# Kernel optimization log

Measured on AMD Instinct MI355X. Metric: run time of the kernel, lower is better.

The kernel has to match this reference:

```python
import jax, jax.numpy as jnp
import numpy as np

B, N_AGENTS, EMBED, HID, N_ACT, S_DIM, O_DIM = 16384, 32, 32, 64, 5, 512, 256


def setup_inputs() -> dict:
    key = jax.random.key(0)
    ks = jax.random.split(key, 12)
    w = lambda k, s: jax.random.normal(k, s, jnp.float32) * 0.05
    return dict(
        states=jax.random.normal(ks[0], (B, S_DIM), jnp.float32),
        agents_obs=jax.random.normal(ks[1], (B, N_AGENTS, O_DIM), jnp.float32),
        fc1_w=w(ks[2], (O_DIM, HID)), fc1_b=jnp.zeros((HID,), jnp.float32),
        fc2_w=w(ks[3], (HID, N_ACT)), fc2_b=jnp.zeros((N_ACT,), jnp.float32),
        hw1_w=w(ks[4], (S_DIM, EMBED * N_AGENTS)), hw1_b=jnp.zeros((EMBED * N_AGENTS,), jnp.float32),
        hb1_w=w(ks[5], (S_DIM, EMBED)), hb1_b=jnp.zeros((EMBED,), jnp.float32),
        hwf_w=w(ks[6], (S_DIM, EMBED)), hwf_b=jnp.zeros((EMBED,), jnp.float32),
        v1_w=w(ks[7], (S_DIM, EMBED)), v1_b=jnp.zeros((EMBED,), jnp.float32),
        v2_w=w(ks[8], (EMBED, 1)), v2_b=jnp.zeros((1,), jnp.float32),
    )


def reference(states, agents_obs, fc1_w, fc1_b, fc2_w, fc2_b,
              hw1_w, hw1_b, hb1_w, hb1_b, hwf_w, hwf_b,
              v1_w, v1_b, v2_w, v2_b):
    # agent network: per-agent Q values [B, N, A]
    x = jax.nn.relu(agents_obs @ fc1_w + fc1_b)
    agents_qs = jax.nn.softmax(x @ fc2_w + fc2_b, axis=-1)

    Bn = states.shape[0]
    # hypernetwork: per-sample mixing weights (non-negative via abs)
    w1 = jnp.abs(states @ hw1_w + hw1_b).reshape(Bn, N_AGENTS, EMBED)  # [B,N,E]
    b1 = states @ hb1_w + hb1_b                                        # [B,E]
    wf = jnp.abs(states @ hwf_w + hwf_b)                               # [B,E]
    v = jax.nn.relu(states @ v1_w + v1_b) @ v2_w + v2_b                # [B,1]

    # chosen (greedy) per-agent Q values
    best_qs = jnp.max(agents_qs, axis=-1)                              # [B,N]

    # batched mixing (replaces the original per-sample python loop)
    y = jax.nn.relu(jnp.einsum('bn,bne->be', best_qs, w1) + b1)        # [B,E]
    q_tot = jnp.einsum('be,be->b', y, wf) + v[:, 0]                    # [B]
    return agents_qs, q_tot
```

## Files before the change

### kernel.cpp

```cpp
#include <hip/hip_runtime.h>
#include <stdint.h>

#define BTOT   16384
#define ROWS_A 524288
#define WT_COLS 1120

#define WT_OFF    0
#define FC1T_OFF  1146880
#define BQ_OFF    1179648

typedef __attribute__((ext_vector_type(8))) short bf8_t;
typedef __attribute__((ext_vector_type(4))) float f4_t;

__device__ __forceinline__ f4_t mfma16(bf8_t a, bf8_t b, f4_t c) {
    return __builtin_amdgcn_mfma_f32_16x16x32_bf16(a, b, c, 0, 0, 0);
}
__device__ __forceinline__ unsigned short f2bf(float f) {
    union { float f; uint32_t u; } x; x.f = f;
    uint32_t r = x.u + 0x7FFFu + ((x.u >> 16) & 1u);
    return (unsigned short)(r >> 16);
}
__device__ __forceinline__ float bf2f(unsigned short h) {
    union { uint32_t u; float f; } x; x.u = ((uint32_t)h) << 16;
    return x.f;
}

__global__ void prep_kernel(const float* __restrict__ fc1_w,
                            const float* __restrict__ hw1_w,
                            const float* __restrict__ hb1_w,
                            const float* __restrict__ hwf_w,
                            const float* __restrict__ v1_w,
                            unsigned short* __restrict__ Wt,
                            unsigned short* __restrict__ fc1t)
{
    int tid = blockIdx.x * 256 + threadIdx.x;
    if (tid < 71680) {
        int e = tid * 8;
        int c = e >> 9, k0 = e & 511;
        const float* src; int N, sc;
        if (c < 1024)      { src = hw1_w; N = 1024; sc = c; }
        else if (c < 1056) { src = hb1_w; N = 32;   sc = c - 1024; }
        else if (c < 1088) { src = hwf_w; N = 32;   sc = c - 1056; }
        else               { src = v1_w;  N = 32;   sc = c - 1088; }
        union { unsigned short s[8]; uint4 v; } pk;
        #pragma unroll
        for (int j = 0; j < 8; ++j) pk.s[j] = f2bf(src[(size_t)(k0 + j) * N + sc]);
        *(uint4*)(Wt + (size_t)c * 512 + k0) = pk.v;
    } else if (tid < 73728) {
        int e = (tid - 71680) * 8;
        int n = e >> 8, k0 = e & 255;
        union { unsigned short s[8]; uint4 v; } pk;
        #pragma unroll
        for (int j = 0; j < 8; ++j) pk.s[j] = f2bf(fc1_w[(size_t)(k0 + j) * 64 + n]);
        *(uint4*)(fc1t + n * 256 + k0) = pk.v;
    }
}

#define A_SB 264
#define A_SA 72
__global__ __launch_bounds__(256, 3)
void agent_kernel(const float* __restrict__ obs,
                  const unsigned short* __restrict__ fc1t,
                  const float* __restrict__ fc1_b,
                  const float* __restrict__ fc2_w,
                  const float* __restrict__ fc2_b,
                  float* __restrict__ out_q,
                  float* __restrict__ bq)
{
    __shared__ unsigned short sB[64 * A_SB];
    __shared__ unsigned short sA[128 * A_SA];
    const int t = threadIdx.x;
    const int R0 = blockIdx.x * 128;
    const int w = t >> 6, lane = t & 63;
    const int c0 = lane & 15, quad = lane >> 4;

    {
        const uint4* src = (const uint4*)fc1t;
        #pragma unroll
        for (int i = 0; i < 8; ++i) {
            int id = t + i * 256;
            int n = id >> 5, off = (id & 31) * 8;
            *(uint4*)(sB + n * A_SB + off) = src[id];
        }
    }

    f4_t acc[2][4];
    #pragma unroll
    for (int mt = 0; mt < 2; ++mt)
        #pragma unroll
        for (int nt = 0; nt < 4; ++nt) acc[mt][nt] = (f4_t){0.f, 0.f, 0.f, 0.f};

    for (int kc = 0; kc < 4; ++kc) {
        __syncthreads();
        #pragma unroll
        for (int i = 0; i < 8; ++i) {
            int id = t + i * 256;
            int row = id >> 4, off = (id & 15) * 4;
            float4 v = *(const float4*)(obs + (size_t)(R0 + row) * 256 + kc * 64 + off);
            ushort4 o; o.x = f2bf(v.x); o.y = f2bf(v.y); o.z = f2bf(v.z); o.w = f2bf(v.w);
            *(ushort4*)(sA + row * A_SA + off) = o;
        }
        __syncthreads();
        #pragma unroll
        for (int ks = 0; ks < 2; ++ks) {
            int kk = ks * 32 + quad * 8;
            bf8_t af[2], bfr[4];
            af[0] = *(const bf8_t*)(sA + (w * 32 + c0) * A_SA + kk);
            af[1] = *(const bf8_t*)(sA + (w * 32 + 16 + c0) * A_SA + kk);
            #pragma unroll
            for (int nt = 0; nt < 4; ++nt)
                bfr[nt] = *(const bf8_t*)(sB + (nt * 16 + c0) * A_SB + kc * 64 + kk);
            #pragma unroll
            for (int mt = 0; mt < 2; ++mt)
                #pragma unroll
                for (int nt = 0; nt < 4; ++nt)
                    acc[mt][nt] = mfma16(af[mt], bfr[nt], acc[mt][nt]);
        }
    }
    __syncthreads();
    unsigned short* xs = sA;
    #pragma unroll
    for (int nt = 0; nt < 4; ++nt) {
        int col = nt * 16 + c0;
        float bias = fc1_b[col];
        #pragma unroll
        for (int mt = 0; mt < 2; ++mt)
            #pragma unroll
            for (int r = 0; r < 4; ++r) {
                int row = w * 32 + mt * 16 + quad * 4 + r;
                float v = acc[mt][nt][r] + bias;
                xs[row * 66 + col] = f2bf(fmaxf(v, 0.f));
            }
    }
    __syncthreads();
    {
        int row = t >> 1, half = t & 1;
        float q[5] = {0.f, 0.f, 0.f, 0.f, 0.f};
        #pragma unroll
        for (int i = 0; i < 32; ++i) {
            int h = half * 32 + i;
            float xv = bf2f(xs[row * 66 + h]);
            #pragma unroll
            for (int j = 0; j < 5; ++j) q[j] += xv * fc2_w[h * 5 + j];
        }
        #pragma unroll
        for (int j = 0; j < 5; ++j) q[j] = q[j] + __shfl_xor(q[j], 1) + fc2_b[j];
        float m = q[0];
        #pragma unroll
        for (int j = 1; j < 5; ++j) m = fmaxf(m, q[j]);
        float e[5], s = 0.f;
        #pragma unroll
        for (int j = 0; j < 5; ++j) { e[j] = __expf(q[j] - m); s += e[j]; }
        float inv = 1.f / s;
        if (half == 0) {
            size_t G = (size_t)R0 + row;
            #pragma unroll
            for (int j = 0; j < 5; ++j) out_q[G * 5 + j] = e[j] * inv;
            bq[G] = inv;
        }
    }
}

#define B_ST 520
__global__ __launch_bounds__(256, 1)
void mixer_kernel(const float* __restrict__ states,
                  const unsigned short* __restrict__ Wt,
                  const float* __restrict__ hw1_b,
                  const float* __restrict__ hb1_b,
                  const float* __restrict__ hwf_b,
                  const float* __restrict__ v1_b,
                  const float* __restrict__ v2_w,
                  const float* __restrict__ v2_b,
                  const float* __restrict__ bq,
                  float* __restrict__ qtot)
{
    extern __shared__ char smem[];
    unsigned short* sA = (unsigned short*)smem;
    unsigned short* sB = (unsigned short*)(smem + 66560);
    float* bqs = (float*)(smem + 133120);
    const int t = threadIdx.x;
    const int B0 = blockIdx.x * 64;
    const int w = t >> 6, lane = t & 63;
    const int c0 = lane & 15, quad = lane >> 4;

    #pragma unroll
    for (int i = 0; i < 32; ++i) {
        int id = t + i * 256;
        int row = id >> 7, off = (id & 127) * 4;
        float4 v = *(const float4*)(states + (size_t)(B0 + row) * 512 + off);
        ushort4 o; o.x = f2bf(v.x); o.y = f2bf(v.y); o.z = f2bf(v.z); o.w = f2bf(v.w);
        *(ushort4*)(sA + row * B_ST + off) = o;
    }
    #pragma unroll
    for (int i = 0; i < 2; ++i) {
        int id = t + i * 256;
        int row = id >> 3, off = (id & 7) * 4;
        float4 v = *(const float4*)(bq + (size_t)(B0 + row) * 32 + off);
        *(float4*)(bqs + row * 36 + off) = v;
    }

    float y_acc[4][2] = {{0.f,0.f},{0.f,0.f},{0.f,0.f},{0.f,0.f}};
    float b1v[4][2], wfv[4][2], vhv[4][2];

    for (int g = 0; g < 18; ++g) {
        __syncthreads();
        int nrows = (g == 17) ? 32 : 64;
        int n0 = g * 64;
        int nv4 = nrows * 64;
        for (int id = t; id < nv4; id += 256) {
            int n = id >> 6, off = (id & 63) * 8;
            *(uint4*)(sB + n * B_ST + off) = *(const uint4*)(Wt + (size_t)(n0 + n) * 512 + off);
        }
        __syncthreads();
        int NT = (g == 17) ? 2 : 4;
        f4_t acc[4];
        #pragma unroll
        for (int nt = 0; nt < 4; ++nt) acc[nt] = (f4_t){0.f, 0.f, 0.f, 0.f};
        for (int ks = 0; ks < 16; ++ks) {
            int kk = ks * 32 + quad * 8;
            bf8_t af = *(const bf8_t*)(sA + (w * 16 + c0) * B_ST + kk);
            for (int nt = 0; nt < NT; ++nt) {
                bf8_t bfr = *(const bf8_t*)(sB + (nt * 16 + c0) * B_ST + kk);
                acc[nt] = mfma16(af, bfr, acc[nt]);
            }
        }
        if (g < 16) {
            #pragma unroll
            for (int nt = 0; nt < 4; ++nt) {
                int colg = n0 + nt * 16 + c0;
                int agent = colg >> 5;
                int eh = nt & 1;
                float bias = hw1_b[colg];
                #pragma unroll
                for (int r = 0; r < 4; ++r) {
                    int rowl = w * 16 + quad * 4 + r;
                    float w1v = fabsf(acc[nt][r] + bias);
                    y_acc[r][eh] += bqs[rowl * 36 + agent] * w1v;
                }
            }
        } else if (g == 16) {
            #pragma unroll
            for (int nt = 0; nt < 2; ++nt) {
                float bias = hb1_b[nt * 16 + c0];
                #pragma unroll
                for (int r = 0; r < 4; ++r) b1v[r][nt] = acc[nt][r] + bias;
            }
            #pragma unroll
            for (int nt = 2; nt < 4; ++nt) {
                float bias = hwf_b[(nt - 2) * 16 + c0];
                #pragma unroll
                for (int r = 0; r < 4; ++r) wfv[r][nt - 2] = fabsf(acc[nt][r] + bias);
            }
        } else {
            #pragma unroll
            for (int nt = 0; nt < 2; ++nt) {
                float bias = v1_b[nt * 16 + c0];
                #pragma unroll
                for (int r = 0; r < 4; ++r) vhv[r][nt] = fmaxf(acc[nt][r] + bias, 0.f);
            }
        }
    }
    float v2w0 = v2_w[c0], v2w1 = v2_w[16 + c0], v2b = v2_b[0];
    float p[4];
    #pragma unroll
    for (int r = 0; r < 4; ++r) {
        float y0 = fmaxf(y_acc[r][0] + b1v[r][0], 0.f);
        float y1 = fmaxf(y_acc[r][1] + b1v[r][1], 0.f);
        p[r] = y0 * wfv[r][0] + y1 * wfv[r][1] + vhv[r][0] * v2w0 + vhv[r][1] * v2w1;
    }
    #pragma unroll
    for (int off = 1; off < 16; off <<= 1)
        #pragma unroll
        for (int r = 0; r < 4; ++r) p[r] += __shfl_xor(p[r], off);
    if (c0 == 0) {
        #pragma unroll
        for (int r = 0; r < 4; ++r)
            qtot[B0 + w * 16 + quad * 4 + r] = p[r] + v2b;
    }
}

extern "C" void kernel_launch(void* const* d_in, const int* in_sizes, int n_in,
                              void* d_out, int out_size, void* d_ws, size_t ws_size,
                              hipStream_t stream) {
    const float* states = (const float*)d_in[0];
    const float* obs    = (const float*)d_in[1];
    const float* fc1_w  = (const float*)d_in[2];
    const float* fc1_b  = (const float*)d_in[3];
    const float* fc2_w  = (const float*)d_in[4];
    const float* fc2_b  = (const float*)d_in[5];
    const float* hw1_w  = (const float*)d_in[6];
    const float* hw1_b  = (const float*)d_in[7];
    const float* hb1_w  = (const float*)d_in[8];
    const float* hb1_b  = (const float*)d_in[9];
    const float* hwf_w  = (const float*)d_in[10];
    const float* hwf_b  = (const float*)d_in[11];
    const float* v1_w   = (const float*)d_in[12];
    const float* v1_b   = (const float*)d_in[13];
    const float* v2_w   = (const float*)d_in[14];
    const float* v2_b   = (const float*)d_in[15];

    unsigned short* Wt   = (unsigned short*)((char*)d_ws + WT_OFF);
    unsigned short* fc1t = (unsigned short*)((char*)d_ws + FC1T_OFF);
    float*          bq   = (float*)((char*)d_ws + BQ_OFF);

    float* out_q = (float*)d_out;
    float* qtot  = out_q + (size_t)ROWS_A * 5;

    prep_kernel<<<288, 256, 0, stream>>>(fc1_w, hw1_w, hb1_w, hwf_w, v1_w, Wt, fc1t);
    agent_kernel<<<ROWS_A / 128, 256, 0, stream>>>(obs, fc1t, fc1_b, fc2_w, fc2_b, out_q, bq);
    (void)hipFuncSetAttribute((const void*)mixer_kernel,
                              hipFuncAttributeMaxDynamicSharedMemorySize, 142336);
    mixer_kernel<<<BTOT / 64, 256, 142336, stream>>>(states, Wt, hw1_b, hb1_b, hwf_b,
                                                     v1_b, v2_w, v2_b, bq, qtot);
}
```

Measured before the change: 982.4 us.

## Load GEMM A operands straight to registers and fuse fc2 epilogue via shuffles

The agent kernel no longer stages observation tiles through shared memory. Each lane loads its A fragment directly from global memory, converts it to bf16 in registers, and computes fc2 plus softmax from the MFMA accumulators using cross-lane shuffle reductions, which removes the LDS round trips and barriers. The mixer kernel keeps the states row in 16 register fragments instead of shared memory, so LDS use drops and two blocks can fit per CU. The weight matrix is zero-padded to 1152 columns so every group runs four tiles without branching. The cost is higher register pressure and uncoalesced strided row loads from global memory.

```diff
diff --git a/kernel.cpp b/kernel.cpp
--- a/kernel.cpp
+++ b/kernel.cpp
@@ -3,11 +3,10 @@
 
 #define BTOT   16384
 #define ROWS_A 524288
-#define WT_COLS 1120
 
 #define WT_OFF    0
-#define FC1T_OFF  1146880
-#define BQ_OFF    1179648
+#define FC1T_OFF  1179648
+#define BQ_OFF    1212416
 
 typedef __attribute__((ext_vector_type(8))) short bf8_t;
 typedef __attribute__((ext_vector_type(4))) float f4_t;
@@ -20,9 +19,11 @@
     uint32_t r = x.u + 0x7FFFu + ((x.u >> 16) & 1u);
     return (unsigned short)(r >> 16);
 }
-__device__ __forceinline__ float bf2f(unsigned short h) {
-    union { uint32_t u; float f; } x; x.u = ((uint32_t)h) << 16;
-    return x.f;
+__device__ __forceinline__ bf8_t cvt8(float4 a, float4 b) {
+    union { unsigned short s[8]; bf8_t v; } u;
+    u.s[0] = f2bf(a.x); u.s[1] = f2bf(a.y); u.s[2] = f2bf(a.z); u.s[3] = f2bf(a.w);
+    u.s[4] = f2bf(b.x); u.s[5] = f2bf(b.y); u.s[6] = f2bf(b.z); u.s[7] = f2bf(b.w);
+    return u.v;
 }
 
 __global__ void prep_kernel(const float* __restrict__ fc1_w,
@@ -34,20 +35,24 @@
                             unsigned short* __restrict__ fc1t)
 {
     int tid = blockIdx.x * 256 + threadIdx.x;
-    if (tid < 71680) {
-        int e = tid * 8;
-        int c = e >> 9, k0 = e & 511;
-        const float* src; int N, sc;
-        if (c < 1024)      { src = hw1_w; N = 1024; sc = c; }
-        else if (c < 1056) { src = hb1_w; N = 32;   sc = c - 1024; }
-        else if (c < 1088) { src = hwf_w; N = 32;   sc = c - 1056; }
-        else               { src = v1_w;  N = 32;   sc = c - 1088; }
+    if (tid < 73728) {
+        int c = tid >> 6;
+        int k0 = (tid & 63) * 8;
         union { unsigned short s[8]; uint4 v; } pk;
-        #pragma unroll
-        for (int j = 0; j < 8; ++j) pk.s[j] = f2bf(src[(size_t)(k0 + j) * N + sc]);
+        if (c < 1120) {
+            const float* src; int N, sc;
+            if (c < 1024)      { src = hw1_w; N = 1024; sc = c; }
+            else if (c < 1056) { src = hb1_w; N = 32;   sc = c - 1024; }
+            else if (c < 1088) { src = hwf_w; N = 32;   sc = c - 1056; }
+            else               { src = v1_w;  N = 32;   sc = c - 1088; }
+            #pragma unroll
+            for (int j = 0; j < 8; ++j) pk.s[j] = f2bf(src[(size_t)(k0 + j) * N + sc]);
+        } else {
+            pk.v = (uint4){0u, 0u, 0u, 0u};
+        }
         *(uint4*)(Wt + (size_t)c * 512 + k0) = pk.v;
-    } else if (tid < 73728) {
-        int e = (tid - 71680) * 8;
+    } else if (tid < 75776) {
+        int e = (tid - 73728) * 8;
         int n = e >> 8, k0 = e & 255;
         union { unsigned short s[8]; uint4 v; } pk;
         #pragma unroll
@@ -57,8 +62,7 @@
 }
 
 #define A_SB 264
-#define A_SA 72
-__global__ __launch_bounds__(256, 3)
+__global__ __launch_bounds__(256, 4)
 void agent_kernel(const float* __restrict__ obs,
                   const unsigned short* __restrict__ fc1t,
                   const float* __restrict__ fc1_b,
@@ -68,9 +72,7 @@
                   float* __restrict__ bq)
 {
     __shared__ unsigned short sB[64 * A_SB];
-    __shared__ unsigned short sA[128 * A_SA];
     const int t = threadIdx.x;
-    const int R0 = blockIdx.x * 128;
     const int w = t >> 6, lane = t & 63;
     const int c0 = lane & 15, quad = lane >> 4;
 
@@ -83,68 +85,67 @@
             *(uint4*)(sB + n * A_SB + off) = src[id];
         }
     }
-
-    f4_t acc[2][4];
-    #pragma unroll
-    for (int mt = 0; mt < 2; ++mt)
-        #pragma unroll
-        for (int nt = 0; nt < 4; ++nt) acc[mt][nt] = (f4_t){0.f, 0.f, 0.f, 0.f};
-
-    for (int kc = 0; kc < 4; ++kc) {
-        __syncthreads();
-        #pragma unroll
-        for (int i = 0; i < 8; ++i) {
-            int id = t + i * 256;
-            int row = id >> 4, off = (id & 15) * 4;
-            float4 v = *(const float4*)(obs + (size_t)(R0 + row) * 256 + kc * 64 + off);
-            ushort4 o; o.x = f2bf(v.x); o.y = f2bf(v.y); o.z = f2bf(v.z); o.w = f2bf(v.w);
-            *(ushort4*)(sA + row * A_SA + off) = o;
-        }
-        __syncthreads();
-        #pragma unroll
-        for (int ks = 0; ks < 2; ++ks) {
+    float b1c[4], w2l[4][5], b2[5];
+    #pragma unroll
+    for (int nt = 0; nt < 4; ++nt) {
+        int h = nt * 16 + c0;
+        b1c[nt] = fc1_b[h];
+        #pragma unroll
+        for (int j = 0; j < 5; ++j) w2l[nt][j] = fc2_w[h * 5 + j];
+    }
+    #pragma unroll
+    for (int j = 0; j < 5; ++j) b2[j] = fc2_b[j];
+    __syncthreads();
+
+    #pragma unroll 1
+    for (int it = 0; it < 4; ++it) {
+        size_t rbase = (size_t)blockIdx.x * 256 + it * 64 + w * 16;
+        const float* arow = obs + (rbase + c0) * 256;
+
+        f4_t acc[4];
+        #pragma unroll
+        for (int nt = 0; nt < 4; ++nt) acc[nt] = (f4_t){0.f, 0.f, 0.f, 0.f};
+
+        #pragma unroll
+        for (int ks = 0; ks < 8; ++ks) {
             int kk = ks * 32 + quad * 8;
-            bf8_t af[2], bfr[4];
-            af[0] = *(const bf8_t*)(sA + (w * 32 + c0) * A_SA + kk);
-            af[1] = *(const bf8_t*)(sA + (w * 32 + 16 + c0) * A_SA + kk);
-            #pragma unroll
-            for (int nt = 0; nt < 4; ++nt)
-                bfr[nt] = *(const bf8_t*)(sB + (nt * 16 + c0) * A_SB + kc * 64 + kk);
-            #pragma unroll
-            for (int mt = 0; mt < 2; ++mt)
-                #pragma unroll
-                for (int nt = 0; nt < 4; ++nt)
-                    acc[mt][nt] = mfma16(af[mt], bfr[nt], acc[mt][nt]);
-        }
-    }
-    __syncthreads();
-    unsigned short* xs = sA;
-    #pragma unroll
-    for (int nt = 0; nt < 4; ++nt) {
-        int col = nt * 16 + c0;
-        float bias = fc1_b[col];
-        #pragma unroll
-        for (int mt = 0; mt < 2; ++mt)
+            float4 a0 = *(const float4*)(arow + kk);
+            float4 a1 = *(const float4*)(arow + kk + 4);
+            bf8_t af = cvt8(a0, a1);
+            #pragma unroll
+            for (int nt = 0; nt < 4; ++nt) {
+                bf8_t bfr = *(const bf8_t*)(sB + (nt * 16 + c0) * A_SB + kk);
+                acc[nt] = mfma16(af, bfr, acc[nt]);
+            }
+        }
+        float p[4][5];
+        #pragma unroll
+        for (int r = 0; r < 4; ++r)
+            #pragma unroll
+            for (int j = 0; j < 5; ++j) p[r][j] = 0.f;
+        #pragma unroll
+        for (int nt = 0; nt < 4; ++nt)
             #pragma unroll
             for (int r = 0; r < 4; ++r) {
-                int row = w * 32 + mt * 16 + quad * 4 + r;
-                float v = acc[mt][nt][r] + bias;
-                xs[row * 66 + col] = f2bf(fmaxf(v, 0.f));
-            }
-    }
-    __syncthreads();
-    {
-        int row = t >> 1, half = t & 1;
-        float q[5] = {0.f, 0.f, 0.f, 0.f, 0.f};
-        #pragma unroll
-        for (int i = 0; i < 32; ++i) {
-            int h = half * 32 + i;
-            float xv = bf2f(xs[row * 66 + h]);
-            #pragma unroll
-            for (int j = 0; j < 5; ++j) q[j] += xv * fc2_w[h * 5 + j];
-        }
-        #pragma unroll
-        for (int j = 0; j < 5; ++j) q[j] = q[j] + __shfl_xor(q[j], 1) + fc2_b[j];
+                float x = fmaxf(acc[nt][r] + b1c[nt], 0.f);
+                #pragma unroll
+                for (int j = 0; j < 5; ++j) p[r][j] += x * w2l[nt][j];
+            }
+        #pragma unroll
+        for (int off = 1; off < 16; off <<= 1)
+            #pragma unroll
+            for (int r = 0; r < 4; ++r)
+                #pragma unroll
+                for (int j = 0; j < 5; ++j) p[r][j] += __shfl_xor(p[r][j], off);
+        float q[5];
+        #pragma unroll
+        for (int j = 0; j < 5; ++j) {
+            float v = p[3][j];
+            v = (c0 == 2) ? p[2][j] : v;
+            v = (c0 == 1) ? p[1][j] : v;
+            v = (c0 == 0) ? p[0][j] : v;
+            q[j] = v + b2[j];
+        }
         float m = q[0];
         #pragma unroll
         for (int j = 1; j < 5; ++j) m = fmaxf(m, q[j]);
@@ -152,8 +153,8 @@
         #pragma unroll
         for (int j = 0; j < 5; ++j) { e[j] = __expf(q[j] - m); s += e[j]; }
         float inv = 1.f / s;
-        if (half == 0) {
-            size_t G = (size_t)R0 + row;
+        if (c0 < 4) {
+            size_t G = rbase + quad * 4 + c0;
             #pragma unroll
             for (int j = 0; j < 5; ++j) out_q[G * 5 + j] = e[j] * inv;
             bq[G] = inv;
@@ -161,8 +162,8 @@
     }
 }
 
-#define B_ST 520
-__global__ __launch_bounds__(256, 1)
+#define M_SB 520
+__global__ __launch_bounds__(256, 2)
 void mixer_kernel(const float* __restrict__ states,
                   const unsigned short* __restrict__ Wt,
                   const float* __restrict__ hw1_b,
@@ -175,59 +176,58 @@
                   float* __restrict__ qtot)
 {
     extern __shared__ char smem[];
-    unsigned short* sA = (unsigned short*)smem;
-    unsigned short* sB = (unsigned short*)(smem + 66560);
-    float* bqs = (float*)(smem + 133120);
+    unsigned short* sB = (unsigned short*)smem;
+    float* bqs = (float*)(smem + 66560);
     const int t = threadIdx.x;
     const int B0 = blockIdx.x * 64;
     const int w = t >> 6, lane = t & 63;
     const int c0 = lane & 15, quad = lane >> 4;
 
     #pragma unroll
-    for (int i = 0; i < 32; ++i) {
-        int id = t + i * 256;
-        int row = id >> 7, off = (id & 127) * 4;
-        float4 v = *(const float4*)(states + (size_t)(B0 + row) * 512 + off);
-        ushort4 o; o.x = f2bf(v.x); o.y = f2bf(v.y); o.z = f2bf(v.z); o.w = f2bf(v.w);
-        *(ushort4*)(sA + row * B_ST + off) = o;
-    }
-    #pragma unroll
     for (int i = 0; i < 2; ++i) {
         int id = t + i * 256;
         int row = id >> 3, off = (id & 7) * 4;
-        float4 v = *(const float4*)(bq + (size_t)(B0 + row) * 32 + off);
-        *(float4*)(bqs + row * 36 + off) = v;
+        *(float4*)(bqs + row * 36 + off) = *(const float4*)(bq + (size_t)(B0 + row) * 32 + off);
+    }
+    const float* srow = states + (size_t)(B0 + w * 16 + c0) * 512;
+    bf8_t areg[16];
+    #pragma unroll
+    for (int ks = 0; ks < 16; ++ks) {
+        int kk = ks * 32 + quad * 8;
+        float4 a0 = *(const float4*)(srow + kk);
+        float4 a1 = *(const float4*)(srow + kk + 4);
+        areg[ks] = cvt8(a0, a1);
     }
 
     float y_acc[4][2] = {{0.f,0.f},{0.f,0.f},{0.f,0.f},{0.f,0.f}};
     float b1v[4][2], wfv[4][2], vhv[4][2];
 
+    #pragma unroll 1
     for (int g = 0; g < 18; ++g) {
         __syncthreads();
-        int nrows = (g == 17) ? 32 : 64;
-        int n0 = g * 64;
-        int nv4 = nrows * 64;
-        for (int id = t; id < nv4; id += 256) {
+        #pragma unroll
+        for (int i = 0; i < 16; ++i) {
+            int id = t + i * 256;
             int n = id >> 6, off = (id & 63) * 8;
-            *(uint4*)(sB + n * B_ST + off) = *(const uint4*)(Wt + (size_t)(n0 + n) * 512 + off);
+            *(uint4*)(sB + n * M_SB + off) = *(const uint4*)(Wt + (size_t)(g * 64 + n) * 512 + off);
         }
         __syncthreads();
-        int NT = (g == 17) ? 2 : 4;
         f4_t acc[4];
         #pragma unroll
         for (int nt = 0; nt < 4; ++nt) acc[nt] = (f4_t){0.f, 0.f, 0.f, 0.f};
+        #pragma unroll
         for (int ks = 0; ks < 16; ++ks) {
             int kk = ks * 32 + quad * 8;
-            bf8_t af = *(const bf8_t*)(sA + (w * 16 + c0) * B_ST + kk);
-            for (int nt = 0; nt < NT; ++nt) {
-                bf8_t bfr = *(const bf8_t*)(sB + (nt * 16 + c0) * B_ST + kk);
-                acc[nt] = mfma16(af, bfr, acc[nt]);
+            #pragma unroll
+            for (int nt = 0; nt < 4; ++nt) {
+                bf8_t bfr = *(const bf8_t*)(sB + (nt * 16 + c0) * M_SB + kk);
+                acc[nt] = mfma16(areg[ks], bfr, acc[nt]);
             }
         }
         if (g < 16) {
             #pragma unroll
             for (int nt = 0; nt < 4; ++nt) {
-                int colg = n0 + nt * 16 + c0;
+                int colg = g * 64 + nt * 16 + c0;
                 int agent = colg >> 5;
                 int eh = nt & 1;
                 float bias = hw1_b[colg];
@@ -288,7 +288,6 @@
     const float* fc1_b  = (const float*)d_in[3];
     const float* fc2_w  = (const float*)d_in[4];
     const float* fc2_b  = (const float*)d_in[5];
-    const float* hw1_w  = (const float*)d_in[6];
     const float* hw1_b  = (const float*)d_in[7];
     const float* hb1_w  = (const float*)d_in[8];
     const float* hb1_b  = (const float*)d_in[9];
@@ -298,6 +297,7 @@
     const float* v1_b   = (const float*)d_in[13];
     const float* v2_w   = (const float*)d_in[14];
     const float* v2_b   = (const float*)d_in[15];
+    const float* hw1_w  = (const float*)d_in[6];
 
     unsigned short* Wt   = (unsigned short*)((char*)d_ws + WT_OFF);
     unsigned short* fc1t = (unsigned short*)((char*)d_ws + FC1T_OFF);
@@ -306,10 +306,10 @@
     float* out_q = (float*)d_out;
     float* qtot  = out_q + (size_t)ROWS_A * 5;
 
-    prep_kernel<<<288, 256, 0, stream>>>(fc1_w, hw1_w, hb1_w, hwf_w, v1_w, Wt, fc1t);
-    agent_kernel<<<ROWS_A / 128, 256, 0, stream>>>(obs, fc1t, fc1_b, fc2_w, fc2_b, out_q, bq);
+    prep_kernel<<<296, 256, 0, stream>>>(fc1_w, hw1_w, hb1_w, hwf_w, v1_w, Wt, fc1t);
+    agent_kernel<<<ROWS_A / 256, 256, 0, stream>>>(obs, fc1t, fc1_b, fc2_w, fc2_b, out_q, bq);
     (void)hipFuncSetAttribute((const void*)mixer_kernel,
-                              hipFuncAttributeMaxDynamicSharedMemorySize, 142336);
-    mixer_kernel<<<BTOT / 64, 256, 142336, stream>>>(states, Wt, hw1_b, hb1_b, hwf_b,
-                                                     v1_b, v2_w, v2_b, bq, qtot);
-}
+                              hipFuncAttributeMaxDynamicSharedMemorySize, 75776);
+    mixer_kernel<<<BTOT / 64, 256, 75776, stream>>>(states, Wt, hw1_b, hb1_b, hwf_b,
+                                                    v1_b, v2_w, v2_b, bq, qtot);
+}
```

Measured after the change: 913.8 us. 7.0% less time.
